# Kernel optimization log

Measured on AMD Instinct MI355X. Metric: run time of the kernel, lower is better.

Reference implementation:

```python
import jax, jax.numpy as jnp
import numpy as np

DIM = 256
HEADS = 8


def _ln(x, g, b, eps=1e-5):
    mu = jnp.mean(x, axis=-1, keepdims=True)
    var = jnp.var(x, axis=-1, keepdims=True)
    return (x - mu) * jax.lax.rsqrt(var + eps) * g + b


def setup_inputs() -> dict:
    key = jax.random.key(0)
    ks = jax.random.split(key, 12)
    d = DIM
    s = lambda fan: 1.0 / np.sqrt(fan)
    return {
        "x": jax.random.normal(ks[0], (1, d, 64, 64), dtype=jnp.float32),
        "ln1_g": jnp.ones((d,), jnp.float32),
        "ln1_b": jnp.zeros((d,), jnp.float32),
        "w_qkv": jax.random.normal(ks[1], (3 * d, d), jnp.float32) * s(d),
        "b_qkv": jnp.zeros((3 * d,), jnp.float32),
        "w_proj": jax.random.normal(ks[2], (d, d), jnp.float32) * s(d),
        "b_proj": jnp.zeros((d,), jnp.float32),
        "ln2_g": jnp.ones((d,), jnp.float32),
        "ln2_b": jnp.zeros((d,), jnp.float32),
        "w_mlp1": jax.random.normal(ks[3], (4 * d, d), jnp.float32) * s(d),
        "b_mlp1": jnp.zeros((4 * d,), jnp.float32),
        "w_mlp2": jax.random.normal(ks[4], (d, 4 * d), jnp.float32) * s(4 * d),
        "b_mlp2": jnp.zeros((d,), jnp.float32),
    }


def reference(x, ln1_g, ln1_b, w_qkv, b_qkv, w_proj, b_proj,
              ln2_g, ln2_b, w_mlp1, b_mlp1, w_mlp2, b_mlp2):
    B, C, H, W = x.shape
    hd = HEADS
    d = C // hd
    scale = d ** (-0.5)
    # work channels-last: [B, H, W, C] -> [B, HW, C]
    xl = jnp.transpose(x, (0, 2, 3, 1)).reshape(B, H * W, C)

    # --- attention branch ---
    xn = _ln(xl, ln1_g, ln1_b)
    qkv = jnp.einsum('bnc,oc->bno', xn, w_qkv) + b_qkv  # [B, N, 3C]
    q, k, v = jnp.split(qkv, 3, axis=-1)
    def heads(t):  # [B,N,C] -> [B,h,N,d]
        return jnp.transpose(t.reshape(B, H * W, hd, d), (0, 2, 1, 3))
    q, k, v = heads(q), heads(k), heads(v)
    attn = jax.nn.softmax(jnp.einsum('bhnd,bhmd->bhnm', q, k) * scale, axis=-1)
    out = jnp.einsum('bhnm,bhmd->bhnd', attn, v)  # [B,h,N,d]
    out = jnp.transpose(out, (0, 2, 1, 3)).reshape(B, H * W, C)
    xl = xl + jnp.einsum('bnc,oc->bno', out, w_proj) + b_proj

    # --- MLP branch ---
    xn = _ln(xl, ln2_g, ln2_b)
    h1 = jax.nn.gelu(jnp.einsum('bnc,oc->bno', xn, w_mlp1) + b_mlp1,
                     approximate=False)
    xl = xl + jnp.einsum('bnf,of->bno', h1, w_mlp2) + b_mlp2

    return jnp.transpose(xl.reshape(B, H, W, C), (0, 3, 1, 2))
```

## Files before the change

### kernel.cpp

```cpp
#include <hip/hip_runtime.h>
#include <hip/hip_bf16.h>

typedef __bf16 bf16_t;
typedef __bf16 bf16x8 __attribute__((ext_vector_type(8)));
typedef __bf16 bf16x4 __attribute__((ext_vector_type(4)));
typedef float  f32x4  __attribute__((ext_vector_type(4)));
typedef unsigned int uint;
typedef uint u32x4 __attribute__((ext_vector_type(4)));

#define MFMA(a,b,c) __builtin_amdgcn_mfma_f32_16x16x32_bf16((a),(b),(c),0,0,0)
#define SPLIT 4

__device__ __forceinline__ size_t pidx(int n, int k, int K) {
  return (size_t)(n >> 4) * (K << 4) + ((k >> 3) << 7) + ((n & 15) << 3) + (k & 7);
}

__device__ __forceinline__ uint packbf2(float lo, float hi) {
  unsigned short a = __builtin_bit_cast(unsigned short, (bf16_t)lo);
  unsigned short b = __builtin_bit_cast(unsigned short, (bf16_t)hi);
  return (uint)a | ((uint)b << 16);
}

__global__ __launch_bounds__(256) void prep(const float* __restrict__ w_qkv,
                                            const float* __restrict__ w_proj,
                                            const float* __restrict__ w_mlp1,
                                            const float* __restrict__ w_mlp2,
                                            bf16_t* __restrict__ wq, bf16_t* __restrict__ wp,
                                            bf16_t* __restrict__ w1, bf16_t* __restrict__ w2,
                                            const float* __restrict__ x,
                                            const float* __restrict__ g,
                                            const float* __restrict__ bta,
                                            float* __restrict__ xl,
                                            bf16_t* __restrict__ xn) {
  __shared__ float tile[256][33];
  __shared__ float psum[8][32], psq[8][32], mu_s[32], rs_s[32];
  int b = blockIdx.x;
  if (b < 384) {
    const float* src; bf16_t* dst; int t0, ksh;
    if (b < 96)       { src = w_qkv;  dst = wq; ksh = 5; t0 = b * 256; }
    else if (b < 128) { src = w_proj; dst = wp; ksh = 5; t0 = (b - 96) * 256; }
    else if (b < 256) { src = w_mlp1; dst = w1; ksh = 5; t0 = (b - 128) * 256; }
    else              { src = w_mlp2; dst = w2; ksh = 7; t0 = (b - 256) * 256; }
    int t = t0 + threadIdx.x;
    int n = t >> ksh, kb = t & ((1 << ksh) - 1);
    int K = 8 << ksh;
    const float* p = src + (size_t)n * K + kb * 8;
    float4 a = *(const float4*)p;
    float4 c = *(const float4*)(p + 4);
    bf16x8 o = {(bf16_t)a.x, (bf16_t)a.y, (bf16_t)a.z, (bf16_t)a.w,
                (bf16_t)c.x, (bf16_t)c.y, (bf16_t)c.z, (bf16_t)c.w};
    *(bf16x8*)(dst + (size_t)(n >> 4) * (K << 4) + kb * 128 + ((n & 15) << 3)) = o;
    return;
  }
  int t = threadIdx.x, n0 = (b - 384) * 32;
  int lane32 = t & 31, grp = t >> 5;
#pragma unroll
  for (int it = 0; it < 32; ++it) {
    int c = grp + it * 8;
    tile[c][lane32] = x[(size_t)c * 4096 + n0 + lane32];
  }
  __syncthreads();
  float s = 0.f, sq = 0.f;
#pragma unroll
  for (int ci = 0; ci < 32; ++ci) {
    float v = tile[grp * 32 + ci][lane32];
    s += v; sq += v * v;
  }
  psum[grp][lane32] = s; psq[grp][lane32] = sq;
  __syncthreads();
  if (t < 32) {
    float S = 0.f, Q = 0.f;
#pragma unroll
    for (int p = 0; p < 8; ++p) { S += psum[p][t]; Q += psq[p][t]; }
    float mu = S * (1.0f / 256.0f);
    float var = Q * (1.0f / 256.0f) - mu * mu;
    mu_s[t] = mu; rs_s[t] = rsqrtf(var + 1e-5f);
  }
  __syncthreads();
  {
    float mu = mu_s[lane32], rs = rs_s[lane32];
    int row = n0 + lane32;
    bf16_t* op = xn + (size_t)(row >> 4) * 4096 + ((row & 15) << 3);
#pragma unroll
    for (int cc8 = 0; cc8 < 4; ++cc8) {
      int c0 = grp * 32 + cc8 * 8;
      bf16x8 o;
#pragma unroll
      for (int j = 0; j < 8; ++j) {
        int c = c0 + j;
        o[j] = (bf16_t)((tile[c][lane32] - mu) * rs * g[c] + bta[c]);
      }
      *(bf16x8*)(op + ((c0 >> 3) << 7)) = o;
    }
  }
#pragma unroll
  for (int it = 0; it < 4; ++it) {
    int j = grp + it * 8;
#pragma unroll
    for (int c0 = 0; c0 < 256; c0 += 32)
      xl[(size_t)(n0 + j) * 256 + c0 + lane32] = tile[c0 + lane32][j];
  }
}

template <int K, int EPI, int RPW, int KS = 1>
__global__ __launch_bounds__(256) void gemm_bt(const bf16_t* __restrict__ A,
                                               const bf16_t* __restrict__ W,
                                               const float* __restrict__ bias,
                                               void* __restrict__ outp, int ldn,
                                               const float* __restrict__ resid) {
  constexpr int RB = RPW / 16;
  constexpr int KLEN = K / KS;
  int w = threadIdx.x >> 6, lane = threadIdx.x & 63;
  int quad = lane >> 4, idx = lane & 15;
  int row0 = blockIdx.x * (4 * RPW) + w * RPW;
  int col0 = blockIdx.y * 64;
  int kb0 = (KS > 1) ? blockIdx.z * KLEN : 0;
  f32x4 acc[RB][4];
#pragma unroll
  for (int rb = 0; rb < RB; ++rb)
#pragma unroll
    for (int nb = 0; nb < 4; ++nb) acc[rb][nb] = (f32x4){0.f, 0.f, 0.f, 0.f};
  const bf16_t* abase = A + (size_t)(row0 >> 4) * (K << 4) + quad * 128 + idx * 8;
  const bf16_t* wbase = W + (size_t)(col0 >> 4) * (K << 4) + quad * 128 + idx * 8;
#pragma unroll 4
  for (int k0 = kb0; k0 < kb0 + KLEN; k0 += 32) {
    bf16x8 a[RB];
#pragma unroll
    for (int rb = 0; rb < RB; ++rb)
      a[rb] = *(const bf16x8*)(abase + (size_t)rb * (K << 4) + k0 * 16);
#pragma unroll
    for (int nb = 0; nb < 4; ++nb) {
      bf16x8 b = *(const bf16x8*)(wbase + (size_t)nb * (K << 4) + k0 * 16);
#pragma unroll
      for (int rb = 0; rb < RB; ++rb) acc[rb][nb] = MFMA(a[rb], b, acc[rb][nb]);
    }
  }
#pragma unroll
  for (int nb = 0; nb < 4; ++nb) {
    int c = col0 + nb * 16 + idx;
    float bv = (EPI == 4) ? 0.f : bias[c];
    if constexpr (EPI == 5) {
      int n = row0 + quad * 4;
      f32x4 o;
#pragma unroll
      for (int r = 0; r < 4; ++r)
        o[r] = acc[0][nb][r] + bv + resid[(size_t)(n + r) * 256 + c];
      *(f32x4*)((float*)outp + (size_t)c * 4096 + n) = o;
    } else {
#pragma unroll
      for (int rb = 0; rb < RB; ++rb)
#pragma unroll
        for (int r = 0; r < 4; ++r) {
          int rr = row0 + rb * 16 + quad * 4 + r;
          float v = acc[rb][nb][r] + bv;
          if constexpr (EPI == 1) {
            float z = v * (0.7978845608f + 0.0356774081f * v * v);
            float t = __builtin_amdgcn_exp2f(z * 2.885390082f);
            float th = 1.f - 2.f * __builtin_amdgcn_rcpf(t + 1.f);
            v = 0.5f * v * (1.f + th);
            ((bf16_t*)outp)[pidx(rr, c, ldn)] = (bf16_t)v;
          } else if constexpr (EPI == 4) {
            ((float*)outp)[((size_t)blockIdx.z * 4096 + rr) * ldn + c] = v;
          } else {
            bf16_t* qh = (bf16_t*)outp;
            bf16_t* kh = qh + 1048576;
            bf16_t* vp = kh + 1048576;
            if (c < 256) {
              qh[(size_t)(c >> 5) * 131072 + rr * 32 + (c & 31)] = (bf16_t)v;
            } else if (c < 512) {
              kh[(size_t)((c - 256) >> 5) * 131072 + rr * 32 + (c & 31)] = (bf16_t)v;
            } else {
              vp[(size_t)((c - 512) >> 5) * 131072 + (rr >> 5) * 1024 + (c & 31) * 32 + (rr & 31)] = (bf16_t)v;
            }
          }
        }
    }
  }
}

__device__ __forceinline__ void quad_transpose(const uint p[4][2], bf16x8& lo, bf16x8& hi) {
  auto sA0 = __builtin_amdgcn_permlane32_swap((int)p[0][0], (int)p[1][0], false, false);
  auto sA1 = __builtin_amdgcn_permlane32_swap((int)p[0][1], (int)p[1][1], false, false);
  auto sB0 = __builtin_amdgcn_permlane16_swap(sA0[0], sA0[1], false, false);
  auto sB1 = __builtin_amdgcn_permlane16_swap(sA1[0], sA1[1], false, false);
  u32x4 w0 = {(uint)sB0[0], (uint)sB1[0], (uint)sB0[1], (uint)sB1[1]};
  lo = __builtin_bit_cast(bf16x8, w0);
  auto tA0 = __builtin_amdgcn_permlane32_swap((int)p[2][0], (int)p[3][0], false, false);
  auto tA1 = __builtin_amdgcn_permlane32_swap((int)p[2][1], (int)p[3][1], false, false);
  auto tB0 = __builtin_amdgcn_permlane16_swap(tA0[0], tA0[1], false, false);
  auto tB1 = __builtin_amdgcn_permlane16_swap(tA1[0], tA1[1], false, false);
  u32x4 w1 = {(uint)tB0[0], (uint)tB1[0], (uint)tB0[1], (uint)tB1[1]};
  hi = __builtin_bit_cast(bf16x8, w1);
}

__global__ __launch_bounds__(256, 4) void attn_split(const bf16_t* __restrict__ qkvh,
                                                     uint* __restrict__ o_part,
                                                     float* __restrict__ l_part) {
  int w = threadIdx.x >> 6, lane = threadIdx.x & 63;
  int quad = lane >> 4, idx = lane & 15;
  int h  = blockIdx.x & 7;
  int qt = (blockIdx.x >> 3) & 31;
  int sp = blockIdx.x >> 8;
  int qrow = qt * 128 + w * 32;
  const bf16_t* qh = qkvh + (size_t)h * 131072;
  const bf16_t* kh = qh + 8 * 131072;
  const bf16_t* vp = kh + 8 * 131072;
  const float cs = 0.25503518f;
  bf16x8 qr0 = *(const bf16x8*)(qh + (size_t)(qrow + idx) * 32 + quad * 8);
  bf16x8 qr1 = *(const bf16x8*)(qh + (size_t)(qrow + 16 + idx) * 32 + quad * 8);
  bf16x8 qf0, qf1;
#pragma unroll
  for (int j = 0; j < 8; ++j) {
    qf0[j] = (bf16_t)((float)qr0[j] * cs);
    qf1[j] = (bf16_t)((float)qr1[j] * cs);
  }
  float ls0 = 0.f, ls1 = 0.f;
  f32x4 o00 = {0.f,0.f,0.f,0.f}, o01 = {0.f,0.f,0.f,0.f};
  f32x4 o10 = {0.f,0.f,0.f,0.f}, o11 = {0.f,0.f,0.f,0.f};
  const f32x4 zero = {0.f,0.f,0.f,0.f};
  int kbase = sp * 1024;

  bf16x8 kf[4];
#pragma unroll
  for (int kb = 0; kb < 4; ++kb)
    kf[kb] = *(const bf16x8*)(kh + (size_t)(kbase + kb * 16 + idx) * 32 + quad * 8);

  for (int kt = 0; kt < 16; ++kt) {
    int k0 = kbase + kt * 64;
    int k1 = kbase + ((kt + 1) & 15) * 64;
    const bf16_t* vt = vp + (size_t)(k0 >> 5) * 1024 + quad * 8;
    bf16x8 vv0 = *(const bf16x8*)(vt + idx * 32);
    bf16x8 vv1 = *(const bf16x8*)(vt + (idx + 16) * 32);
    bf16x8 vv2 = *(const bf16x8*)(vt + 1024 + idx * 32);
    bf16x8 vv3 = *(const bf16x8*)(vt + 1024 + (idx + 16) * 32);
    bf16x8 kfn[4];
#pragma unroll
    for (int kb = 0; kb < 4; ++kb)
      kfn[kb] = *(const bf16x8*)(kh + (size_t)(k1 + kb * 16 + idx) * 32 + quad * 8);
    __builtin_amdgcn_s_setprio(1);
    uint p0[4][2], p1[4][2];
#pragma unroll
    for (int kb = 0; kb < 4; ++kb) {
      f32x4 s0 = MFMA(kf[kb], qf0, zero);
      f32x4 s1 = MFMA(kf[kb], qf1, zero);
      float a0 = __builtin_amdgcn_exp2f(s0[0]), a1 = __builtin_amdgcn_exp2f(s0[1]);
      float a2 = __builtin_amdgcn_exp2f(s0[2]), a3 = __builtin_amdgcn_exp2f(s0[3]);
      float b0 = __builtin_amdgcn_exp2f(s1[0]), b1 = __builtin_amdgcn_exp2f(s1[1]);
      float b2 = __builtin_amdgcn_exp2f(s1[2]), b3 = __builtin_amdgcn_exp2f(s1[3]);
      ls0 += (a0 + a1) + (a2 + a3);
      ls1 += (b0 + b1) + (b2 + b3);
      p0[kb][0] = packbf2(a0, a1); p0[kb][1] = packbf2(a2, a3);
      p1[kb][0] = packbf2(b0, b1); p1[kb][1] = packbf2(b2, b3);
    }
    bf16x8 pa0, pa1, pb0, pb1;
    quad_transpose(p0, pa0, pa1);
    quad_transpose(p1, pb0, pb1);
    o00 = MFMA(pa0, vv0, o00);
    o01 = MFMA(pa0, vv1, o01);
    o10 = MFMA(pb0, vv0, o10);
    o11 = MFMA(pb0, vv1, o11);
    o00 = MFMA(pa1, vv2, o00);
    o01 = MFMA(pa1, vv3, o01);
    o10 = MFMA(pb1, vv2, o10);
    o11 = MFMA(pb1, vv3, o11);
    __builtin_amdgcn_s_setprio(0);
#pragma unroll
    for (int kb = 0; kb < 4; ++kb) kf[kb] = kfn[kb];
  }
  ls0 += __shfl_xor(ls0, 16); ls0 += __shfl_xor(ls0, 32);
  ls1 += __shfl_xor(ls1, 16); ls1 += __shfl_xor(ls1, 32);
  if (quad == 0) {
    l_part[((size_t)sp * 8 + h) * 4096 + qrow + idx]      = ls0;
    l_part[((size_t)sp * 8 + h) * 4096 + qrow + 16 + idx] = ls1;
  }
#pragma unroll
  for (int r = 0; r < 4; ++r) {
    int n0 = qrow + quad * 4 + r;
    o_part[(((size_t)sp * 4096 + n0) * 8 + h) * 16 + idx] = packbf2(o00[r], o01[r]);
    int n1 = n0 + 16;
    o_part[(((size_t)sp * 4096 + n1) * 8 + h) * 16 + idx] = packbf2(o10[r], o11[r]);
  }
}

__global__ __launch_bounds__(256) void attn_norm(const uint* __restrict__ o_part,
                                                 const float* __restrict__ l_part,
                                                 bf16_t* __restrict__ attn) {
  int t = blockIdx.x * 256 + threadIdx.x;
  int j0 = (t & 3) * 4;
  int h  = (t >> 2) & 7;
  int n  = t >> 5;
  float l = 0.f;
#pragma unroll
  for (int s = 0; s < SPLIT; ++s) l += l_part[((size_t)s * 8 + h) * 4096 + n];
  float inv = 1.0f / l;
  float alo[4] = {0.f,0.f,0.f,0.f}, ahi[4] = {0.f,0.f,0.f,0.f};
#pragma unroll
  for (int s = 0; s < SPLIT; ++s) {
    const uint* p = o_part + (((size_t)s * 4096 + n) * 8 + h) * 16 + j0;
    uint4 v = *(const uint4*)p;
    uint vv[4] = {v.x, v.y, v.z, v.w};
#pragma unroll
    for (int jj = 0; jj < 4; ++jj) {
      alo[jj] += __builtin_bit_cast(float, vv[jj] << 16);
      ahi[jj] += __builtin_bit_cast(float, vv[jj] & 0xffff0000u);
    }
  }
  bf16x4 lo = {(bf16_t)(alo[0] * inv), (bf16_t)(alo[1] * inv),
               (bf16_t)(alo[2] * inv), (bf16_t)(alo[3] * inv)};
  bf16x4 hi = {(bf16_t)(ahi[0] * inv), (bf16_t)(ahi[1] * inv),
               (bf16_t)(ahi[2] * inv), (bf16_t)(ahi[3] * inv)};
  int k1 = h * 32 + j0;
  int k2 = k1 + 16;
  *(bf16x4*)(attn + (size_t)(n >> 4) * 4096 + ((k1 >> 3) << 7) + ((n & 15) << 3) + (k1 & 7)) = lo;
  *(bf16x4*)(attn + (size_t)(n >> 4) * 4096 + ((k2 >> 3) << 7) + ((n & 15) << 3) + (k2 & 7)) = hi;
}

__global__ __launch_bounds__(256) void combine_ln(const float* __restrict__ pp,
                                                  const float* __restrict__ xl,
                                                  const float* __restrict__ bias,
                                                  const float* __restrict__ g,
                                                  const float* __restrict__ bta,
                                                  float* __restrict__ xl2,
                                                  bf16_t* __restrict__ xn2) {
  int row  = blockIdx.x * 4 + (threadIdx.x >> 6);
  int lane = threadIdx.x & 63;
  size_t ri = (size_t)row * 64 + lane;
  float4 rr = ((const float4*)xl)[ri];
  float4 bb = ((const float4*)bias)[lane];
  float4 v = {rr.x + bb.x, rr.y + bb.y, rr.z + bb.z, rr.w + bb.w};
#pragma unroll
  for (int s = 0; s < 2; ++s) {
    float4 p = ((const float4*)pp)[ri + (size_t)s * 4096 * 64];
    v.x += p.x; v.y += p.y; v.z += p.z; v.w += p.w;
  }
  ((float4*)xl2)[ri] = v;
  float s  = v.x + v.y + v.z + v.w;
  float sq = v.x * v.x + v.y * v.y + v.z * v.z + v.w * v.w;
#pragma unroll
  for (int off = 32; off; off >>= 1) {
    s  += __shfl_xor(s, off);
    sq += __shfl_xor(sq, off);
  }
  float mu  = s * (1.0f / 256.0f);
  float var = sq * (1.0f / 256.0f) - mu * mu;
  float rs  = rsqrtf(var + 1e-5f);
  float4 gg = ((const float4*)g)[lane];
  float4 b2 = ((const float4*)bta)[lane];
  bf16x4 o = {(bf16_t)((v.x - mu) * rs * gg.x + b2.x),
              (bf16_t)((v.y - mu) * rs * gg.y + b2.y),
              (bf16_t)((v.z - mu) * rs * gg.z + b2.z),
              (bf16_t)((v.w - mu) * rs * gg.w + b2.w)};
  int k = lane * 4;
  *(bf16x4*)(xn2 + (size_t)(row >> 4) * 4096 + ((k >> 3) << 7) + ((row & 15) << 3) + (k & 7)) = o;
}

extern "C" void kernel_launch(void* const* d_in, const int* in_sizes, int n_in,
                              void* d_out, int out_size, void* d_ws, size_t ws_size,
                              hipStream_t stream) {
  const float* x      = (const float*)d_in[0];
  const float* ln1_g  = (const float*)d_in[1];
  const float* ln1_b  = (const float*)d_in[2];
  const float* w_qkv  = (const float*)d_in[3];
  const float* b_qkv  = (const float*)d_in[4];
  const float* w_proj = (const float*)d_in[5];
  const float* b_proj = (const float*)d_in[6];
  const float* ln2_g  = (const float*)d_in[7];
  const float* ln2_b  = (const float*)d_in[8];
  const float* w_mlp1 = (const float*)d_in[9];
  const float* b_mlp1 = (const float*)d_in[10];
  const float* w_mlp2 = (const float*)d_in[11];
  const float* b_mlp2 = (const float*)d_in[12];

  char* ws = (char*)d_ws;
  bf16_t* qkvh   = (bf16_t*)(ws + 0);
  float*  xl     = (float*)(ws + (6u << 20));
  bf16_t* xn     = (bf16_t*)(ws + (10u << 20));
  uint*   o_part = (uint*)(ws + (12u << 20));
  bf16_t* attn   = (bf16_t*)(ws + (20u << 20));
  float*  pp     = (float*)(ws + (24u << 20));
  float*  xl2    = (float*)(ws + (10u << 20));
  bf16_t* xn2    = (bf16_t*)(ws + (14u << 20));
  bf16_t* h1     = (bf16_t*)(ws + 0);
  bf16_t* wq     = (bf16_t*)(ws + (32u << 20));
  bf16_t* wp     = wq + 196608;
  bf16_t* w1     = wp + 65536;
  bf16_t* w2     = w1 + 262144;
  float*  l_part = (float*)(ws + (34304u << 10));

  prep<<<512, 256, 0, stream>>>(w_qkv, w_proj, w_mlp1, w_mlp2, wq, wp, w1, w2,
                                x, ln1_g, ln1_b, xl, xn);

  gemm_bt<256, 3, 16><<<dim3(64, 12), 256, 0, stream>>>(xn, wq, b_qkv, qkvh, 768, nullptr);
  attn_split<<<256 * SPLIT, 256, 0, stream>>>(qkvh, o_part, l_part);
  attn_norm<<<512, 256, 0, stream>>>(o_part, l_part, attn);

  gemm_bt<256, 4, 16, 2><<<dim3(64, 4, 2), 256, 0, stream>>>(attn, wp, nullptr, pp, 256, nullptr);
  combine_ln<<<1024, 256, 0, stream>>>(pp, xl, b_proj, ln2_g, ln2_b, xl2, xn2);

  gemm_bt<256, 1, 16><<<dim3(64, 16), 256, 0, stream>>>(xn2, w1, b_mlp1, h1, 1024, nullptr);
  gemm_bt<1024, 5, 16, 1><<<dim3(64, 4), 256, 0, stream>>>(h1, w2, b_mlp2, d_out, 256, xl2);
}
```

Before: 163.9 us.

## Fuse proj GEMM with residual+LayerNorm epilogue and compute softmax sums via MFMA

```diff
diff --git a/kernel.cpp b/kernel.cpp
--- a/kernel.cpp
+++ b/kernel.cpp
@@ -107,13 +107,17 @@
                                                const bf16_t* __restrict__ W,
                                                const float* __restrict__ bias,
                                                void* __restrict__ outp, int ldn,
-                                               const float* __restrict__ resid) {
+                                               const float* __restrict__ resid,
+                                               const float* __restrict__ g2,
+                                               const float* __restrict__ bt2,
+                                               bf16_t* __restrict__ xn2p) {
   constexpr int RB = RPW / 16;
   constexpr int KLEN = K / KS;
   int w = threadIdx.x >> 6, lane = threadIdx.x & 63;
   int quad = lane >> 4, idx = lane & 15;
-  int row0 = blockIdx.x * (4 * RPW) + w * RPW;
-  int col0 = blockIdx.y * 64;
+  int row0, col0;
+  if constexpr (EPI == 6) { row0 = blockIdx.x * 16; col0 = w * 64; }
+  else { row0 = blockIdx.x * (4 * RPW) + w * RPW; col0 = blockIdx.y * 64; }
   int kb0 = (KS > 1) ? blockIdx.z * KLEN : 0;
   f32x4 acc[RB][4];
 #pragma unroll
@@ -135,6 +139,69 @@
       for (int rb = 0; rb < RB; ++rb) acc[rb][nb] = MFMA(a[rb], b, acc[rb][nb]);
     }
   }
+
+  if constexpr (EPI == 6) {
+    __shared__ float lns[4][2][16];
+    __shared__ bf16_t tile[16][256];
+    float vv[4][4];
+    float ps[4] = {0.f, 0.f, 0.f, 0.f}, pq[4] = {0.f, 0.f, 0.f, 0.f};
+#pragma unroll
+    for (int nb = 0; nb < 4; ++nb) {
+      int c = col0 + nb * 16 + idx;
+      float bv = bias[c];
+#pragma unroll
+      for (int r = 0; r < 4; ++r) {
+        int rr = row0 + quad * 4 + r;
+        float t = acc[0][nb][r] + bv + resid[(size_t)rr * 256 + c];
+        vv[nb][r] = t;
+        ((float*)outp)[(size_t)rr * 256 + c] = t;
+        ps[r] += t; pq[r] += t * t;
+      }
+    }
+#pragma unroll
+    for (int m = 1; m < 16; m <<= 1)
+#pragma unroll
+      for (int r = 0; r < 4; ++r) {
+        ps[r] += __shfl_xor(ps[r], m);
+        pq[r] += __shfl_xor(pq[r], m);
+      }
+    if (idx == 0)
+#pragma unroll
+      for (int r = 0; r < 4; ++r) {
+        lns[w][0][quad * 4 + r] = ps[r];
+        lns[w][1][quad * 4 + r] = pq[r];
+      }
+    __syncthreads();
+    float mu[4], rs[4];
+#pragma unroll
+    for (int r = 0; r < 4; ++r) {
+      int row = quad * 4 + r;
+      float S = (lns[0][0][row] + lns[1][0][row]) + (lns[2][0][row] + lns[3][0][row]);
+      float Q = (lns[0][1][row] + lns[1][1][row]) + (lns[2][1][row] + lns[3][1][row]);
+      float m_ = S * (1.0f / 256.0f);
+      mu[r] = m_;
+      rs[r] = rsqrtf(Q * (1.0f / 256.0f) - m_ * m_ + 1e-5f);
+    }
+#pragma unroll
+    for (int nb = 0; nb < 4; ++nb) {
+      int c = col0 + nb * 16 + idx;
+      float gg = g2[c], bb = bt2[c];
+#pragma unroll
+      for (int r = 0; r < 4; ++r)
+        tile[quad * 4 + r][c] = (bf16_t)((vv[nb][r] - mu[r]) * rs[r] * gg + bb);
+    }
+    __syncthreads();
+    {
+      int t = threadIdx.x;
+      int row = t >> 4, k0 = (t & 15) * 16;
+      int grr = row0 + row;
+      bf16_t* op = xn2p + (size_t)(grr >> 4) * 4096 + ((grr & 15) << 3);
+      *(bf16x8*)(op + ((k0 >> 3) << 7)) = *(const bf16x8*)&tile[row][k0];
+      *(bf16x8*)(op + (((k0 + 8) >> 3) << 7)) = *(const bf16x8*)&tile[row][k0 + 8];
+    }
+    return;
+  }
+
 #pragma unroll
   for (int nb = 0; nb < 4; ++nb) {
     int c = col0 + nb * 16 + idx;
@@ -208,15 +275,16 @@
   const float cs = 0.25503518f;
   bf16x8 qr0 = *(const bf16x8*)(qh + (size_t)(qrow + idx) * 32 + quad * 8);
   bf16x8 qr1 = *(const bf16x8*)(qh + (size_t)(qrow + 16 + idx) * 32 + quad * 8);
-  bf16x8 qf0, qf1;
+  bf16x8 qf0, qf1, ones1;
 #pragma unroll
   for (int j = 0; j < 8; ++j) {
     qf0[j] = (bf16_t)((float)qr0[j] * cs);
     qf1[j] = (bf16_t)((float)qr1[j] * cs);
-  }
-  float ls0 = 0.f, ls1 = 0.f;
+    ones1[j] = (bf16_t)1.0f;
+  }
   f32x4 o00 = {0.f,0.f,0.f,0.f}, o01 = {0.f,0.f,0.f,0.f};
   f32x4 o10 = {0.f,0.f,0.f,0.f}, o11 = {0.f,0.f,0.f,0.f};
+  f32x4 lsA = {0.f,0.f,0.f,0.f}, lsB = {0.f,0.f,0.f,0.f};
   const f32x4 zero = {0.f,0.f,0.f,0.f};
   int kbase = sp * 1024;
 
@@ -247,8 +315,6 @@
       float a2 = __builtin_amdgcn_exp2f(s0[2]), a3 = __builtin_amdgcn_exp2f(s0[3]);
       float b0 = __builtin_amdgcn_exp2f(s1[0]), b1 = __builtin_amdgcn_exp2f(s1[1]);
       float b2 = __builtin_amdgcn_exp2f(s1[2]), b3 = __builtin_amdgcn_exp2f(s1[3]);
-      ls0 += (a0 + a1) + (a2 + a3);
-      ls1 += (b0 + b1) + (b2 + b3);
       p0[kb][0] = packbf2(a0, a1); p0[kb][1] = packbf2(a2, a3);
       p1[kb][0] = packbf2(b0, b1); p1[kb][1] = packbf2(b2, b3);
     }
@@ -259,19 +325,25 @@
     o01 = MFMA(pa0, vv1, o01);
     o10 = MFMA(pb0, vv0, o10);
     o11 = MFMA(pb0, vv1, o11);
+    lsA = MFMA(pa0, ones1, lsA);
+    lsB = MFMA(pb0, ones1, lsB);
     o00 = MFMA(pa1, vv2, o00);
     o01 = MFMA(pa1, vv3, o01);
     o10 = MFMA(pb1, vv2, o10);
     o11 = MFMA(pb1, vv3, o11);
+    lsA = MFMA(pa1, ones1, lsA);
+    lsB = MFMA(pb1, ones1, lsB);
     __builtin_amdgcn_s_setprio(0);
 #pragma unroll
     for (int kb = 0; kb < 4; ++kb) kf[kb] = kfn[kb];
   }
-  ls0 += __shfl_xor(ls0, 16); ls0 += __shfl_xor(ls0, 32);
-  ls1 += __shfl_xor(ls1, 16); ls1 += __shfl_xor(ls1, 32);
-  if (quad == 0) {
-    l_part[((size_t)sp * 8 + h) * 4096 + qrow + idx]      = ls0;
-    l_part[((size_t)sp * 8 + h) * 4096 + qrow + 16 + idx] = ls1;
+  if (idx == 0) {
+    float* lp = l_part + ((size_t)sp * 8 + h) * 4096 + qrow;
+#pragma unroll
+    for (int r = 0; r < 4; ++r) {
+      lp[quad * 4 + r]      = lsA[r];
+      lp[16 + quad * 4 + r] = lsB[r];
+    }
   }
 #pragma unroll
   for (int r = 0; r < 4; ++r) {
@@ -313,45 +385,6 @@
   int k2 = k1 + 16;
   *(bf16x4*)(attn + (size_t)(n >> 4) * 4096 + ((k1 >> 3) << 7) + ((n & 15) << 3) + (k1 & 7)) = lo;
   *(bf16x4*)(attn + (size_t)(n >> 4) * 4096 + ((k2 >> 3) << 7) + ((n & 15) << 3) + (k2 & 7)) = hi;
-}
-
-__global__ __launch_bounds__(256) void combine_ln(const float* __restrict__ pp,
-                                                  const float* __restrict__ xl,
-                                                  const float* __restrict__ bias,
-                                                  const float* __restrict__ g,
-                                                  const float* __restrict__ bta,
-                                                  float* __restrict__ xl2,
-                                                  bf16_t* __restrict__ xn2) {
-  int row  = blockIdx.x * 4 + (threadIdx.x >> 6);
-  int lane = threadIdx.x & 63;
-  size_t ri = (size_t)row * 64 + lane;
-  float4 rr = ((const float4*)xl)[ri];
-  float4 bb = ((const float4*)bias)[lane];
-  float4 v = {rr.x + bb.x, rr.y + bb.y, rr.z + bb.z, rr.w + bb.w};
-#pragma unroll
-  for (int s = 0; s < 2; ++s) {
-    float4 p = ((const float4*)pp)[ri + (size_t)s * 4096 * 64];
-    v.x += p.x; v.y += p.y; v.z += p.z; v.w += p.w;
-  }
-  ((float4*)xl2)[ri] = v;
-  float s  = v.x + v.y + v.z + v.w;
-  float sq = v.x * v.x + v.y * v.y + v.z * v.z + v.w * v.w;
-#pragma unroll
-  for (int off = 32; off; off >>= 1) {
-    s  += __shfl_xor(s, off);
-    sq += __shfl_xor(sq, off);
-  }
-  float mu  = s * (1.0f / 256.0f);
-  float var = sq * (1.0f / 256.0f) - mu * mu;
-  float rs  = rsqrtf(var + 1e-5f);
-  float4 gg = ((const float4*)g)[lane];
-  float4 b2 = ((const float4*)bta)[lane];
-  bf16x4 o = {(bf16_t)((v.x - mu) * rs * gg.x + b2.x),
-              (bf16_t)((v.y - mu) * rs * gg.y + b2.y),
-              (bf16_t)((v.z - mu) * rs * gg.z + b2.z),
-              (bf16_t)((v.w - mu) * rs * gg.w + b2.w)};
-  int k = lane * 4;
-  *(bf16x4*)(xn2 + (size_t)(row >> 4) * 4096 + ((k >> 3) << 7) + ((row & 15) << 3) + (k & 7)) = o;
 }
 
 extern "C" void kernel_launch(void* const* d_in, const int* in_sizes, int n_in,
@@ -377,7 +410,6 @@
   bf16_t* xn     = (bf16_t*)(ws + (10u << 20));
   uint*   o_part = (uint*)(ws + (12u << 20));
   bf16_t* attn   = (bf16_t*)(ws + (20u << 20));
-  float*  pp     = (float*)(ws + (24u << 20));
   float*  xl2    = (float*)(ws + (10u << 20));
   bf16_t* xn2    = (bf16_t*)(ws + (14u << 20));
   bf16_t* h1     = (bf16_t*)(ws + 0);
@@ -390,13 +422,16 @@
   prep<<<512, 256, 0, stream>>>(w_qkv, w_proj, w_mlp1, w_mlp2, wq, wp, w1, w2,
                                 x, ln1_g, ln1_b, xl, xn);
 
-  gemm_bt<256, 3, 16><<<dim3(64, 12), 256, 0, stream>>>(xn, wq, b_qkv, qkvh, 768, nullptr);
+  gemm_bt<256, 3, 16><<<dim3(64, 12), 256, 0, stream>>>(
+      xn, wq, b_qkv, qkvh, 768, nullptr, nullptr, nullptr, nullptr);
   attn_split<<<256 * SPLIT, 256, 0, stream>>>(qkvh, o_part, l_part);
   attn_norm<<<512, 256, 0, stream>>>(o_part, l_part, attn);
 
-  gemm_bt<256, 4, 16, 2><<<dim3(64, 4, 2), 256, 0, stream>>>(attn, wp, nullptr, pp, 256, nullptr);
-  combine_ln<<<1024, 256, 0, stream>>>(pp, xl, b_proj, ln2_g, ln2_b, xl2, xn2);
-
-  gemm_bt<256, 1, 16><<<dim3(64, 16), 256, 0, stream>>>(xn2, w1, b_mlp1, h1, 1024, nullptr);
-  gemm_bt<1024, 5, 16, 1><<<dim3(64, 4), 256, 0, stream>>>(h1, w2, b_mlp2, d_out, 256, xl2);
-}
+  gemm_bt<256, 6, 16, 1><<<256, 256, 0, stream>>>(
+      attn, wp, b_proj, xl2, 256, xl, ln2_g, ln2_b, xn2);
+
+  gemm_bt<256, 1, 16><<<dim3(64, 16), 256, 0, stream>>>(
+      xn2, w1, b_mlp1, h1, 1024, nullptr, nullptr, nullptr, nullptr);
+  gemm_bt<1024, 5, 16, 1><<<dim3(64, 4), 256, 0, stream>>>(
+      h1, w2, b_mlp2, d_out, 256, xl2, nullptr, nullptr, nullptr);
+}
```

Measured after the change: 163.8 us, median of 2. About the same (-0.0%).
